# Performance work log

Measured on AMD Instinct MI355X. Metric: run time of the kernel, lower is better.

## Reference

```python
import jax, jax.numpy as jnp
import numpy as np

B, S, D, H = 64, 512, 256, 512

def setup_inputs() -> dict:
    key = jax.random.key(0)
    ks = jax.random.split(key, 16)
    s_in = 1.0 / np.sqrt(D)
    s_h = 1.0 / np.sqrt(H)
    inp = {
        "inputs": jax.random.normal(ks[0], (B, S, D), jnp.float32),
        # input-side gate weights (stored [D,H], equiv to torch Linear weight.T)
        "Wf": jax.random.uniform(ks[1], (D, H), jnp.float32, -s_in, s_in),
        "Wi": jax.random.uniform(ks[2], (D, H), jnp.float32, -s_in, s_in),
        "Wo": jax.random.uniform(ks[3], (D, H), jnp.float32, -s_in, s_in),
        "Wc": jax.random.uniform(ks[4], (D, H), jnp.float32, -s_in, s_in),
        "bf": jax.random.uniform(ks[5], (H,), jnp.float32, -s_in, s_in),
        "bi": jax.random.uniform(ks[6], (H,), jnp.float32, -s_in, s_in),
        "bo": jax.random.uniform(ks[7], (H,), jnp.float32, -s_in, s_in),
        "bc": jax.random.uniform(ks[8], (H,), jnp.float32, -s_in, s_in),
        # recurrent weights (bias=False)
        "Uf": jax.random.uniform(ks[9], (H, H), jnp.float32, -s_h, s_h),
        "Ui": jax.random.uniform(ks[10], (H, H), jnp.float32, -s_h, s_h),
        "Uo": jax.random.uniform(ks[11], (H, H), jnp.float32, -s_h, s_h),
        "Uc": jax.random.uniform(ks[12], (H, H), jnp.float32, -s_h, s_h),
        # output head
        "Wfc": jax.random.uniform(ks[13], (H, 1), jnp.float32, -s_h, s_h),
        "bfc": jax.random.uniform(ks[14], (1,), jnp.float32, -s_h, s_h),
    }
    return inp


def reference(inputs, Wf, Wi, Wo, Wc, bf, bi, bo, bc, Uf, Ui, Uo, Uc, Wfc, bfc):
    # Precompute all input-side gate projections in one big GEMM: [B,S,4H]
    Wx = jnp.concatenate([Wf, Wi, Wo, Wc], axis=1)            # [D,4H]
    bx = jnp.concatenate([bf, bi, bo, bc], axis=0)            # [4H]
    gx = jnp.einsum('bsd,dg->bsg', inputs, Wx) + bx           # [B,S,4H]
    Uh = jnp.concatenate([Uf, Ui, Uo, Uc], axis=1)            # [H,4H]

    h0 = jnp.zeros((inputs.shape[0], Uf.shape[0]), inputs.dtype)
    c0 = jnp.zeros_like(h0)
    Hd = Uf.shape[0]

    def step(carry, gx_t):
        h, c = carry
        g = gx_t + h @ Uh                                     # [B,4H]
        f_t = jax.nn.sigmoid(g[:, 0 * Hd:1 * Hd])
        i_t = jax.nn.sigmoid(g[:, 1 * Hd:2 * Hd])
        o_t = jax.nn.sigmoid(g[:, 2 * Hd:3 * Hd])
        chat = jnp.tanh(g[:, 3 * Hd:4 * Hd])
        c = f_t * c + i_t * chat
        h = o_t * jnp.tanh(c)
        return (h, c), h

    (h_t, c_t), hs = jax.lax.scan(step, (h0, c0), jnp.swapaxes(gx, 0, 1))
    outputs = jnp.swapaxes(hs, 0, 1)                          # [B,S,H]
    predictions = jnp.einsum('bsh,ho->bso', outputs, Wfc) + bfc
    return predictions, h_t, c_t
```

## Files before the change

### kernel.cpp

```cpp
#include <hip/hip_runtime.h>
#include <hip/hip_bf16.h>

#define B_ 64
#define S_ 512
#define D_ 256
#define H_ 512

typedef __attribute__((ext_vector_type(8))) short bf16x8;
typedef __attribute__((ext_vector_type(4))) float f32x4;
typedef __attribute__((ext_vector_type(4))) unsigned int uint4v;
typedef unsigned short ushort_t;
typedef unsigned long long u64_t;

__device__ __forceinline__ ushort_t f2bf(float f) {
    __hip_bfloat16 h = __float2bfloat16(f);
    return *reinterpret_cast<ushort_t*>(&h);
}
__device__ __forceinline__ float sigmoid_f(float x) { return 1.f / (1.f + __expf(-x)); }
__device__ __forceinline__ float tanh_f(float x) { return 1.f - 2.f / (__expf(2.f * x) + 1.f); }

__device__ __forceinline__ void lds_barrier() {
    asm volatile("s_waitcnt lgkmcnt(0)\n\ts_barrier" ::: "memory");
}

__global__ __launch_bounds__(512, 2) void lstm_rec(
    const float* __restrict__ X,
    const float* __restrict__ Wf, const float* __restrict__ Wi,
    const float* __restrict__ Wo, const float* __restrict__ Wc,
    const float* __restrict__ bfp, const float* __restrict__ bip,
    const float* __restrict__ bop, const float* __restrict__ bcp,
    const float* __restrict__ Uf, const float* __restrict__ Ui,
    const float* __restrict__ Uo, const float* __restrict__ Uc,
    const float* __restrict__ Wfc,
    float* __restrict__ pred, u64_t* __restrict__ hbuf,
    unsigned int* __restrict__ xcdtab,
    float* __restrict__ outH, float* __restrict__ outC)
{
    __shared__ ushort_t hS[16 * 520];
    __shared__ ushort_t xS[16 * 264];
    __shared__ float gact[4][16][68];
    __shared__ int meta[2];

    const int tid  = threadIdx.x;
    const int w    = tid >> 6;
    const int lane = tid & 63;
    const int q    = lane >> 4;
    const int m    = lane & 15;
    const int gate = w >> 1;
    const int half = w & 1;

    if (w == 0) {
        unsigned int xcd;
        asm volatile("s_getreg_b32 %0, hwreg(HW_REG_XCC_ID)" : "=s"(xcd));
        xcd &= 15u;
        if (lane == 0)
            __hip_atomic_store(&xcdtab[blockIdx.x], xcd + 1u,
                               __ATOMIC_RELEASE, __HIP_MEMORY_SCOPE_AGENT);
        unsigned int entry;
        for (;;) {
            entry = __hip_atomic_load(&xcdtab[lane], __ATOMIC_ACQUIRE, __HIP_MEMORY_SCOPE_AGENT);
            if (__ballot(entry != 0u) == ~0ull) break;
            __builtin_amdgcn_s_sleep(1);
        }
        const unsigned int xcd_j = entry - 1u;
        const unsigned int key_j = (xcd_j << 8) | (unsigned int)lane;
        const unsigned int mykey = (xcd << 8) | (unsigned int)blockIdx.x;
        const int rank = __popcll(__ballot(key_j < mykey));
        const int c_lt = __popcll(__ballot(xcd_j < xcd));
        const int c_eq = __popcll(__ballot(xcd_j == xcd));
        const int gg   = rank >> 3;
        const bool uni = (c_lt <= gg * 8) && (gg * 8 + 8 <= c_lt + c_eq);
        if (lane == 0) { meta[0] = rank; meta[1] = uni ? 1 : 0; }
    }
    __syncthreads();
    const int  rank    = meta[0];
    const bool uniform = meta[1] != 0;
    if (rank >= 32) return;
    const int g = rank >> 3;
    const int s = rank & 7;

    const int ncol0 = s * 64 + half * 32 + m;
    const int ncol1 = ncol0 + 16;

    const float* Ug = (gate == 0) ? Uf : (gate == 1) ? Ui : (gate == 2) ? Uo : Uc;
    const float* Wg = (gate == 0) ? Wf : (gate == 1) ? Wi : (gate == 2) ? Wo : Wc;
    const float* bg = (gate == 0) ? bfp : (gate == 1) ? bip : (gate == 2) ? bop : bcp;

    const float bias0 = bg[ncol0];
    const float bias1 = bg[ncol1];

    bf16x8 UF[2][16];
    bf16x8 WF[2][8];
    #pragma unroll
    for (int tt = 0; tt < 2; ++tt) {
        const int nc = tt ? ncol1 : ncol0;
        #pragma unroll
        for (int ks = 0; ks < 16; ++ks) {
            bf16x8 v;
            #pragma unroll
            for (int j = 0; j < 8; ++j)
                v[j] = (short)f2bf(Ug[(ks * 32 + q * 8 + j) * H_ + nc]);
            UF[tt][ks] = v;
        }
        #pragma unroll
        for (int ks = 0; ks < 8; ++ks) {
            bf16x8 v;
            #pragma unroll
            for (int j = 0; j < 8; ++j)
                v[j] = (short)f2bf(Wg[(ks * 32 + q * 8 + j) * H_ + nc]);
            WF[tt][ks] = v;
        }
    }

    const int urow  = tid >> 5;
    const int upair = tid & 31;
    const float2 wfc2 = *(const float2*)&Wfc[s * 64 + 2 * upair];

    float cr0 = 0.f, cr1 = 0.f;

    {
        const float* xsrc = &X[((size_t)(g * 16 + urow) * S_ + 0) * D_ + upair * 8];
        float4 a = *(const float4*)xsrc;
        float4 b = *(const float4*)(xsrc + 4);
        bf16x8 v;
        v[0] = (short)f2bf(a.x); v[1] = (short)f2bf(a.y);
        v[2] = (short)f2bf(a.z); v[3] = (short)f2bf(a.w);
        v[4] = (short)f2bf(b.x); v[5] = (short)f2bf(b.y);
        v[6] = (short)f2bf(b.z); v[7] = (short)f2bf(b.w);
        *(bf16x8*)&xS[urow * 264 + upair * 8] = v;
    }

    float4 xr0, xr1;

    for (int t = 0; t < S_; ++t) {
        {
            const int row = tid >> 5;
            const int pr  = (tid & 31) * 8;
            u64_t* pe = hbuf + ((size_t)((t & 1) * B_ + g * 16 + row) * 256 + pr);
            const unsigned int tg = (unsigned int)t;
            uint4v ra, rb;
            bool got = false;
            if (uniform) {
                uint4v r0, r1, r2, r3;
                asm volatile(
                    "global_load_dwordx4 %0, %4, off sc0\n\t"
                    "global_load_dwordx4 %1, %5, off sc0\n\t"
                    "global_load_dwordx4 %2, %6, off sc0\n\t"
                    "global_load_dwordx4 %3, %7, off sc0\n\t"
                    "s_waitcnt vmcnt(0)"
                    : "=v"(r0), "=v"(r1), "=v"(r2), "=v"(r3)
                    : "v"(pe), "v"(pe + 2), "v"(pe + 4), "v"(pe + 6)
                    : "memory");
                bool ok = r0[1] == tg && r0[3] == tg && r1[1] == tg && r1[3] == tg
                       && r2[1] == tg && r2[3] == tg && r3[1] == tg && r3[3] == tg;
                if (__ballot(ok) == ~0ull) {
                    ra[0] = r0[0]; ra[1] = r0[2]; ra[2] = r1[0]; ra[3] = r1[2];
                    rb[0] = r2[0]; rb[1] = r2[2]; rb[2] = r3[0]; rb[3] = r3[2];
                    got = true;
                }
            }
            if (!got) {
                for (;;) {
                    u64_t e0 = __hip_atomic_load(pe + 0, __ATOMIC_RELAXED, __HIP_MEMORY_SCOPE_AGENT);
                    u64_t e1 = __hip_atomic_load(pe + 1, __ATOMIC_RELAXED, __HIP_MEMORY_SCOPE_AGENT);
                    u64_t e2 = __hip_atomic_load(pe + 2, __ATOMIC_RELAXED, __HIP_MEMORY_SCOPE_AGENT);
                    u64_t e3 = __hip_atomic_load(pe + 3, __ATOMIC_RELAXED, __HIP_MEMORY_SCOPE_AGENT);
                    u64_t e4 = __hip_atomic_load(pe + 4, __ATOMIC_RELAXED, __HIP_MEMORY_SCOPE_AGENT);
                    u64_t e5 = __hip_atomic_load(pe + 5, __ATOMIC_RELAXED, __HIP_MEMORY_SCOPE_AGENT);
                    u64_t e6 = __hip_atomic_load(pe + 6, __ATOMIC_RELAXED, __HIP_MEMORY_SCOPE_AGENT);
                    u64_t e7 = __hip_atomic_load(pe + 7, __ATOMIC_RELAXED, __HIP_MEMORY_SCOPE_AGENT);
                    bool ok = (unsigned int)(e0 >> 32) == tg && (unsigned int)(e1 >> 32) == tg
                           && (unsigned int)(e2 >> 32) == tg && (unsigned int)(e3 >> 32) == tg
                           && (unsigned int)(e4 >> 32) == tg && (unsigned int)(e5 >> 32) == tg
                           && (unsigned int)(e6 >> 32) == tg && (unsigned int)(e7 >> 32) == tg;
                    if (__ballot(ok) == ~0ull) {
                        ra[0] = (unsigned int)e0; ra[1] = (unsigned int)e1;
                        ra[2] = (unsigned int)e2; ra[3] = (unsigned int)e3;
                        rb[0] = (unsigned int)e4; rb[1] = (unsigned int)e5;
                        rb[2] = (unsigned int)e6; rb[3] = (unsigned int)e7;
                        break;
                    }
                    __builtin_amdgcn_s_sleep(1);
                }
            }
            if (t + 1 < S_) {
                const float* xsrc = &X[((size_t)(g * 16 + urow) * S_ + (t + 1)) * D_ + upair * 8];
                xr0 = *(const float4*)xsrc;
                xr1 = *(const float4*)(xsrc + 4);
            }
            *(uint4v*)&hS[row * 520 + pr * 2]     = ra;
            *(uint4v*)&hS[row * 520 + pr * 2 + 8] = rb;
        }
        lds_barrier();

        f32x4 accA0 = {bias0, bias0, bias0, bias0};
        f32x4 accA1 = {bias1, bias1, bias1, bias1};
        f32x4 accB0 = {0.f, 0.f, 0.f, 0.f};
        f32x4 accB1 = {0.f, 0.f, 0.f, 0.f};
        #pragma unroll
        for (int ks = 0; ks < 8; ++ks) {
            bf16x8 a = *(const bf16x8*)&xS[m * 264 + ks * 32 + q * 8];
            accA0 = __builtin_amdgcn_mfma_f32_16x16x32_bf16(a, WF[0][ks], accA0, 0, 0, 0);
            accA1 = __builtin_amdgcn_mfma_f32_16x16x32_bf16(a, WF[1][ks], accA1, 0, 0, 0);
        }
        #pragma unroll
        for (int ks = 0; ks < 16; ++ks) {
            bf16x8 a = *(const bf16x8*)&hS[m * 520 + ks * 32 + q * 8];
            accB0 = __builtin_amdgcn_mfma_f32_16x16x32_bf16(a, UF[0][ks], accB0, 0, 0, 0);
            accB1 = __builtin_amdgcn_mfma_f32_16x16x32_bf16(a, UF[1][ks], accB1, 0, 0, 0);
        }
        #pragma unroll
        for (int j = 0; j < 4; ++j) {
            float v0 = accA0[j] + accB0[j];
            float v1 = accA1[j] + accB1[j];
            v0 = (gate < 3) ? sigmoid_f(v0) : tanh_f(v0);
            v1 = (gate < 3) ? sigmoid_f(v1) : tanh_f(v1);
            gact[gate][q * 4 + j][half * 32 + m]      = v0;
            gact[gate][q * 4 + j][half * 32 + 16 + m] = v1;
        }
        lds_barrier();

        float2 f2v = *(const float2*)&gact[0][urow][2 * upair];
        float2 i2v = *(const float2*)&gact[1][urow][2 * upair];
        float2 o2v = *(const float2*)&gact[2][urow][2 * upair];
        float2 ch2 = *(const float2*)&gact[3][urow][2 * upair];
        cr0 = f2v.x * cr0 + i2v.x * ch2.x;
        cr1 = f2v.y * cr1 + i2v.y * ch2.y;
        float hv0 = o2v.x * tanh_f(cr0);
        float hv1 = o2v.y * tanh_f(cr1);

        if (t < S_ - 1) {
            unsigned int packed = (unsigned int)f2bf(hv0) | ((unsigned int)f2bf(hv1) << 16);
            u64_t ent = ((u64_t)(unsigned int)(t + 1) << 32) | (u64_t)packed;
            u64_t* hdst = hbuf + ((size_t)(((t + 1) & 1) * B_ + g * 16 + urow) * 256
                                  + s * 32 + upair);
            asm volatile("global_store_dwordx2 %0, %1, off sc0 sc1"
                         :: "v"(hdst), "v"(ent) : "memory");
            bf16x8 v;
            v[0] = (short)f2bf(xr0.x); v[1] = (short)f2bf(xr0.y);
            v[2] = (short)f2bf(xr0.z); v[3] = (short)f2bf(xr0.w);
            v[4] = (short)f2bf(xr1.x); v[5] = (short)f2bf(xr1.y);
            v[6] = (short)f2bf(xr1.z); v[7] = (short)f2bf(xr1.w);
            *(bf16x8*)&xS[urow * 264 + upair * 8] = v;
        } else {
            *(float2*)&outH[(g * 16 + urow) * H_ + s * 64 + 2 * upair] = make_float2(hv0, hv1);
            *(float2*)&outC[(g * 16 + urow) * H_ + s * 64 + 2 * upair] = make_float2(cr0, cr1);
        }

        float pv = hv0 * wfc2.x + hv1 * wfc2.y;
        pv += __shfl_xor(pv, 16);
        pv += __shfl_xor(pv, 8);
        pv += __shfl_xor(pv, 4);
        pv += __shfl_xor(pv, 2);
        pv += __shfl_xor(pv, 1);
        if (upair == 0) atomicAdd(&pred[(g * 16 + urow) * S_ + t], pv);
    }
}

__global__ void pred_fin(const float* __restrict__ pred,
                         const float* __restrict__ bfc,
                         float* __restrict__ out)
{
    int i = blockIdx.x * blockDim.x + threadIdx.x;
    if (i < B_ * S_) out[i] = pred[i] + bfc[0];
}

extern "C" void kernel_launch(void* const* d_in, const int* in_sizes, int n_in,
                              void* d_out, int out_size, void* d_ws, size_t ws_size,
                              hipStream_t stream) {
    const float* X   = (const float*)d_in[0];
    const float* Wf  = (const float*)d_in[1];
    const float* Wi  = (const float*)d_in[2];
    const float* Wo  = (const float*)d_in[3];
    const float* Wc  = (const float*)d_in[4];
    const float* bfp = (const float*)d_in[5];
    const float* bip = (const float*)d_in[6];
    const float* bop = (const float*)d_in[7];
    const float* bcp = (const float*)d_in[8];
    const float* Uf  = (const float*)d_in[9];
    const float* Ui  = (const float*)d_in[10];
    const float* Uo  = (const float*)d_in[11];
    const float* Uc  = (const float*)d_in[12];
    const float* Wfc = (const float*)d_in[13];
    const float* bfc = (const float*)d_in[14];

    float*        pred   = (float*)d_ws;
    u64_t*        hbuf   = (u64_t*)((char*)d_ws + 131072);
    unsigned int* xcdtab = (unsigned int*)((char*)d_ws + 393216);

    hipMemsetAsync(d_ws, 0, 393216 + 256, stream);

    float* out = (float*)d_out;
    lstm_rec<<<64, 512, 0, stream>>>(X, Wf, Wi, Wo, Wc, bfp, bip, bop, bcp,
                                     Uf, Ui, Uo, Uc, Wfc,
                                     pred, hbuf, xcdtab,
                                     out + 32768, out + 65536);
    pred_fin<<<128, 256, 0, stream>>>(pred, bfc, out);
}
```

Measured before the change: 2.231 ms.

## Process all four batch groups per block on eight co-located blocks

Instead of 32 active blocks (4 batch groups × 8 hidden slices), only 8 blocks stay active and each loops over all four 16-row batch groups per timestep, with separate LDS buffers per group. The intent is to keep all cooperating blocks on one XCD so cross-block h exchange stays in a shared cache and the fast uniform load path is taken more often. In exchange each block does four times the serial work per step with more barriers, and the uniform flag now requires the eight lowest-ranked blocks to share the lowest XCD.

```diff
diff --git a/kernel.cpp b/kernel.cpp
--- a/kernel.cpp
+++ b/kernel.cpp
@@ -23,7 +23,7 @@
     asm volatile("s_waitcnt lgkmcnt(0)\n\ts_barrier" ::: "memory");
 }
 
-__global__ __launch_bounds__(512, 2) void lstm_rec(
+__global__ __launch_bounds__(512) void lstm_rec(
     const float* __restrict__ X,
     const float* __restrict__ Wf, const float* __restrict__ Wi,
     const float* __restrict__ Wo, const float* __restrict__ Wc,
@@ -36,9 +36,8 @@
     unsigned int* __restrict__ xcdtab,
     float* __restrict__ outH, float* __restrict__ outC)
 {
-    __shared__ ushort_t hS[16 * 520];
-    __shared__ ushort_t xS[16 * 264];
-    __shared__ float gact[4][16][68];
+    __shared__ __attribute__((aligned(16))) unsigned char blob[4][17408];
+    __shared__ ushort_t xS[4][16 * 264];
     __shared__ int meta[2];
 
     const int tid  = threadIdx.x;
@@ -68,16 +67,14 @@
         const int rank = __popcll(__ballot(key_j < mykey));
         const int c_lt = __popcll(__ballot(xcd_j < xcd));
         const int c_eq = __popcll(__ballot(xcd_j == xcd));
-        const int gg   = rank >> 3;
-        const bool uni = (c_lt <= gg * 8) && (gg * 8 + 8 <= c_lt + c_eq);
+        const bool uni = (c_lt == 0) && (c_eq >= 8);
         if (lane == 0) { meta[0] = rank; meta[1] = uni ? 1 : 0; }
     }
     __syncthreads();
     const int  rank    = meta[0];
     const bool uniform = meta[1] != 0;
-    if (rank >= 32) return;
-    const int g = rank >> 3;
-    const int s = rank & 7;
+    if (rank >= 8) return;
+    const int s = rank;
 
     const int ncol0 = s * 64 + half * 32 + m;
     const int ncol1 = ncol0 + 16;
@@ -116,10 +113,12 @@
     const int upair = tid & 31;
     const float2 wfc2 = *(const float2*)&Wfc[s * 64 + 2 * upair];
 
-    float cr0 = 0.f, cr1 = 0.f;
-
-    {
-        const float* xsrc = &X[((size_t)(g * 16 + urow) * S_ + 0) * D_ + upair * 8];
+    float cr0[4] = {0.f, 0.f, 0.f, 0.f};
+    float cr1[4] = {0.f, 0.f, 0.f, 0.f};
+
+    #pragma unroll
+    for (int gi = 0; gi < 4; ++gi) {
+        const float* xsrc = &X[((size_t)(gi * 16 + urow) * S_ + 0) * D_ + upair * 8];
         float4 a = *(const float4*)xsrc;
         float4 b = *(const float4*)(xsrc + 4);
         bf16x8 v;
@@ -127,133 +126,140 @@
         v[2] = (short)f2bf(a.z); v[3] = (short)f2bf(a.w);
         v[4] = (short)f2bf(b.x); v[5] = (short)f2bf(b.y);
         v[6] = (short)f2bf(b.z); v[7] = (short)f2bf(b.w);
-        *(bf16x8*)&xS[urow * 264 + upair * 8] = v;
+        *(bf16x8*)&xS[gi][urow * 264 + upair * 8] = v;
     }
 
-    float4 xr0, xr1;
-
     for (int t = 0; t < S_; ++t) {
-        {
-            const int row = tid >> 5;
-            const int pr  = (tid & 31) * 8;
-            u64_t* pe = hbuf + ((size_t)((t & 1) * B_ + g * 16 + row) * 256 + pr);
-            const unsigned int tg = (unsigned int)t;
-            uint4v ra, rb;
-            bool got = false;
-            if (uniform) {
-                uint4v r0, r1, r2, r3;
-                asm volatile(
-                    "global_load_dwordx4 %0, %4, off sc0\n\t"
-                    "global_load_dwordx4 %1, %5, off sc0\n\t"
-                    "global_load_dwordx4 %2, %6, off sc0\n\t"
-                    "global_load_dwordx4 %3, %7, off sc0\n\t"
-                    "s_waitcnt vmcnt(0)"
-                    : "=v"(r0), "=v"(r1), "=v"(r2), "=v"(r3)
-                    : "v"(pe), "v"(pe + 2), "v"(pe + 4), "v"(pe + 6)
-                    : "memory");
-                bool ok = r0[1] == tg && r0[3] == tg && r1[1] == tg && r1[3] == tg
-                       && r2[1] == tg && r2[3] == tg && r3[1] == tg && r3[3] == tg;
-                if (__ballot(ok) == ~0ull) {
-                    ra[0] = r0[0]; ra[1] = r0[2]; ra[2] = r1[0]; ra[3] = r1[2];
-                    rb[0] = r2[0]; rb[1] = r2[2]; rb[2] = r3[0]; rb[3] = r3[2];
-                    got = true;
+        #pragma unroll
+        for (int gi = 0; gi < 4; ++gi) {
+            ushort_t* hS = (ushort_t*)blob[gi];
+            float*    ga = (float*)blob[gi];
+            float4 xr0, xr1;
+
+            {
+                const int row = tid >> 5;
+                const int pr  = (tid & 31) * 8;
+                u64_t* pe = hbuf + ((size_t)((t & 1) * B_ + gi * 16 + row) * 256 + pr);
+                const unsigned int tg = (unsigned int)t;
+                uint4v ra, rb;
+                bool got = false;
+                if (uniform) {
+                    uint4v r0, r1, r2, r3;
+                    asm volatile(
+                        "global_load_dwordx4 %0, %4, off sc0\n\t"
+                        "global_load_dwordx4 %1, %5, off sc0\n\t"
+                        "global_load_dwordx4 %2, %6, off sc0\n\t"
+                        "global_load_dwordx4 %3, %7, off sc0\n\t"
+                        "s_waitcnt vmcnt(0)"
+                        : "=v"(r0), "=v"(r1), "=v"(r2), "=v"(r3)
+                        : "v"(pe), "v"(pe + 2), "v"(pe + 4), "v"(pe + 6)
+                        : "memory");
+                    bool ok = r0[1] == tg && r0[3] == tg && r1[1] == tg && r1[3] == tg
+                           && r2[1] == tg && r2[3] == tg && r3[1] == tg && r3[3] == tg;
+                    if (__ballot(ok) == ~0ull) {
+                        ra[0] = r0[0]; ra[1] = r0[2]; ra[2] = r1[0]; ra[3] = r1[2];
+                        rb[0] = r2[0]; rb[1] = r2[2]; rb[2] = r3[0]; rb[3] = r3[2];
+                        got = true;
+                    }
                 }
-            }
-            if (!got) {
-                for (;;) {
-                    u64_t e0 = __hip_atomic_load(pe + 0, __ATOMIC_RELAXED, __HIP_MEMORY_SCOPE_AGENT);
-                    u64_t e1 = __hip_atomic_load(pe + 1, __ATOMIC_RELAXED, __HIP_MEMORY_SCOPE_AGENT);
-                    u64_t e2 = __hip_atomic_load(pe + 2, __ATOMIC_RELAXED, __HIP_MEMORY_SCOPE_AGENT);
-                    u64_t e3 = __hip_atomic_load(pe + 3, __ATOMIC_RELAXED, __HIP_MEMORY_SCOPE_AGENT);
-                    u64_t e4 = __hip_atomic_load(pe + 4, __ATOMIC_RELAXED, __HIP_MEMORY_SCOPE_AGENT);
-                    u64_t e5 = __hip_atomic_load(pe + 5, __ATOMIC_RELAXED, __HIP_MEMORY_SCOPE_AGENT);
-                    u64_t e6 = __hip_atomic_load(pe + 6, __ATOMIC_RELAXED, __HIP_MEMORY_SCOPE_AGENT);
-                    u64_t e7 = __hip_atomic_load(pe + 7, __ATOMIC_RELAXED, __HIP_MEMORY_SCOPE_AGENT);
-                    bool ok = (unsigned int)(e0 >> 32) == tg && (unsigned int)(e1 >> 32) == tg
-                           && (unsigned int)(e2 >> 32) == tg && (unsigned int)(e3 >> 32) == tg
-                           && (unsigned int)(e4 >> 32) == tg && (unsigned int)(e5 >> 32) == tg
-                           && (unsigned int)(e6 >> 32) == tg && (unsigned int)(e7 >> 32) == tg;
-                    if (__ballot(ok) == ~0ull) {
-                        ra[0] = (unsigned int)e0; ra[1] = (unsigned int)e1;
-                        ra[2] = (unsigned int)e2; ra[3] = (unsigned int)e3;
-                        rb[0] = (unsigned int)e4; rb[1] = (unsigned int)e5;
-                        rb[2] = (unsigned int)e6; rb[3] = (unsigned int)e7;
-                        break;
+                if (!got) {
+                    for (;;) {
+                        u64_t e0 = __hip_atomic_load(pe + 0, __ATOMIC_RELAXED, __HIP_MEMORY_SCOPE_AGENT);
+                        u64_t e1 = __hip_atomic_load(pe + 1, __ATOMIC_RELAXED, __HIP_MEMORY_SCOPE_AGENT);
+                        u64_t e2 = __hip_atomic_load(pe + 2, __ATOMIC_RELAXED, __HIP_MEMORY_SCOPE_AGENT);
+                        u64_t e3 = __hip_atomic_load(pe + 3, __ATOMIC_RELAXED, __HIP_MEMORY_SCOPE_AGENT);
+                        u64_t e4 = __hip_atomic_load(pe + 4, __ATOMIC_RELAXED, __HIP_MEMORY_SCOPE_AGENT);
+                        u64_t e5 = __hip_atomic_load(pe + 5, __ATOMIC_RELAXED, __HIP_MEMORY_SCOPE_AGENT);
+                        u64_t e6 = __hip_atomic_load(pe + 6, __ATOMIC_RELAXED, __HIP_MEMORY_SCOPE_AGENT);
+                        u64_t e7 = __hip_atomic_load(pe + 7, __ATOMIC_RELAXED, __HIP_MEMORY_SCOPE_AGENT);
+                        bool ok = (unsigned int)(e0 >> 32) == tg && (unsigned int)(e1 >> 32) == tg
+                               && (unsigned int)(e2 >> 32) == tg && (unsigned int)(e3 >> 32) == tg
+                               && (unsigned int)(e4 >> 32) == tg && (unsigned int)(e5 >> 32) == tg
+                               && (unsigned int)(e6 >> 32) == tg && (unsigned int)(e7 >> 32) == tg;
+                        if (__ballot(ok) == ~0ull) {
+                            ra[0] = (unsigned int)e0; ra[1] = (unsigned int)e1;
+                            ra[2] = (unsigned int)e2; ra[3] = (unsigned int)e3;
+                            rb[0] = (unsigned int)e4; rb[1] = (unsigned int)e5;
+                            rb[2] = (unsigned int)e6; rb[3] = (unsigned int)e7;
+                            break;
+                        }
+                        __builtin_amdgcn_s_sleep(1);
                     }
-                    __builtin_amdgcn_s_sleep(1);
                 }
-            }
-            if (t + 1 < S_) {
-                const float* xsrc = &X[((size_t)(g * 16 + urow) * S_ + (t + 1)) * D_ + upair * 8];
-                xr0 = *(const float4*)xsrc;
-                xr1 = *(const float4*)(xsrc + 4);
-            }
-            *(uint4v*)&hS[row * 520 + pr * 2]     = ra;
-            *(uint4v*)&hS[row * 520 + pr * 2 + 8] = rb;
+                if (t + 1 < S_) {
+                    const float* xs2 = &X[((size_t)(gi * 16 + urow) * S_ + (t + 1)) * D_ + upair * 8];
+                    xr0 = *(const float4*)xs2;
+                    xr1 = *(const float4*)(xs2 + 4);
+                }
+                *(uint4v*)&hS[row * 520 + pr * 2]     = ra;
+                *(uint4v*)&hS[row * 520 + pr * 2 + 8] = rb;
+            }
+            lds_barrier();
+
+            f32x4 accA0 = {bias0, bias0, bias0, bias0};
+            f32x4 accA1 = {bias1, bias1, bias1, bias1};
+            f32x4 accB0 = {0.f, 0.f, 0.f, 0.f};
+            f32x4 accB1 = {0.f, 0.f, 0.f, 0.f};
+            #pragma unroll
+            for (int ks = 0; ks < 8; ++ks) {
+                bf16x8 a = *(const bf16x8*)&xS[gi][m * 264 + ks * 32 + q * 8];
+                accA0 = __builtin_amdgcn_mfma_f32_16x16x32_bf16(a, WF[0][ks], accA0, 0, 0, 0);
+                accA1 = __builtin_amdgcn_mfma_f32_16x16x32_bf16(a, WF[1][ks], accA1, 0, 0, 0);
+            }
+            #pragma unroll
+            for (int ks = 0; ks < 16; ++ks) {
+                bf16x8 a = *(const bf16x8*)&hS[m * 520 + ks * 32 + q * 8];
+                accB0 = __builtin_amdgcn_mfma_f32_16x16x32_bf16(a, UF[0][ks], accB0, 0, 0, 0);
+                accB1 = __builtin_amdgcn_mfma_f32_16x16x32_bf16(a, UF[1][ks], accB1, 0, 0, 0);
+            }
+            lds_barrier();
+
+            #pragma unroll
+            for (int j = 0; j < 4; ++j) {
+                float v0 = accA0[j] + accB0[j];
+                float v1 = accA1[j] + accB1[j];
+                v0 = (gate < 3) ? sigmoid_f(v0) : tanh_f(v0);
+                v1 = (gate < 3) ? sigmoid_f(v1) : tanh_f(v1);
+                ga[((size_t)gate * 16 + q * 4 + j) * 68 + half * 32 + m]      = v0;
+                ga[((size_t)gate * 16 + q * 4 + j) * 68 + half * 32 + 16 + m] = v1;
+            }
+            lds_barrier();
+
+            float2 f2v = *(const float2*)&ga[((size_t)0 * 16 + urow) * 68 + 2 * upair];
+            float2 i2v = *(const float2*)&ga[((size_t)1 * 16 + urow) * 68 + 2 * upair];
+            float2 o2v = *(const float2*)&ga[((size_t)2 * 16 + urow) * 68 + 2 * upair];
+            float2 ch2 = *(const float2*)&ga[((size_t)3 * 16 + urow) * 68 + 2 * upair];
+            cr0[gi] = f2v.x * cr0[gi] + i2v.x * ch2.x;
+            cr1[gi] = f2v.y * cr1[gi] + i2v.y * ch2.y;
+            float hv0 = o2v.x * tanh_f(cr0[gi]);
+            float hv1 = o2v.y * tanh_f(cr1[gi]);
+
+            if (t < S_ - 1) {
+                unsigned int packed = (unsigned int)f2bf(hv0) | ((unsigned int)f2bf(hv1) << 16);
+                u64_t ent = ((u64_t)(unsigned int)(t + 1) << 32) | (u64_t)packed;
+                u64_t* hdst = hbuf + ((size_t)(((t + 1) & 1) * B_ + gi * 16 + urow) * 256
+                                      + s * 32 + upair);
+                asm volatile("global_store_dwordx2 %0, %1, off sc0 sc1"
+                             :: "v"(hdst), "v"(ent) : "memory");
+                bf16x8 v;
+                v[0] = (short)f2bf(xr0.x); v[1] = (short)f2bf(xr0.y);
+                v[2] = (short)f2bf(xr0.z); v[3] = (short)f2bf(xr0.w);
+                v[4] = (short)f2bf(xr1.x); v[5] = (short)f2bf(xr1.y);
+                v[6] = (short)f2bf(xr1.z); v[7] = (short)f2bf(xr1.w);
+                *(bf16x8*)&xS[gi][urow * 264 + upair * 8] = v;
+            } else {
+                *(float2*)&outH[(gi * 16 + urow) * H_ + s * 64 + 2 * upair] = make_float2(hv0, hv1);
+                *(float2*)&outC[(gi * 16 + urow) * H_ + s * 64 + 2 * upair] = make_float2(cr0[gi], cr1[gi]);
+            }
+
+            float pv = hv0 * wfc2.x + hv1 * wfc2.y;
+            pv += __shfl_xor(pv, 16);
+            pv += __shfl_xor(pv, 8);
+            pv += __shfl_xor(pv, 4);
+            pv += __shfl_xor(pv, 2);
+            pv += __shfl_xor(pv, 1);
+            if (upair == 0) atomicAdd(&pred[(gi * 16 + urow) * S_ + t], pv);
         }
-        lds_barrier();
-
-        f32x4 accA0 = {bias0, bias0, bias0, bias0};
-        f32x4 accA1 = {bias1, bias1, bias1, bias1};
-        f32x4 accB0 = {0.f, 0.f, 0.f, 0.f};
-        f32x4 accB1 = {0.f, 0.f, 0.f, 0.f};
-        #pragma unroll
-        for (int ks = 0; ks < 8; ++ks) {
-            bf16x8 a = *(const bf16x8*)&xS[m * 264 + ks * 32 + q * 8];
-            accA0 = __builtin_amdgcn_mfma_f32_16x16x32_bf16(a, WF[0][ks], accA0, 0, 0, 0);
-            accA1 = __builtin_amdgcn_mfma_f32_16x16x32_bf16(a, WF[1][ks], accA1, 0, 0, 0);
-        }
-        #pragma unroll
-        for (int ks = 0; ks < 16; ++ks) {
-            bf16x8 a = *(const bf16x8*)&hS[m * 520 + ks * 32 + q * 8];
-            accB0 = __builtin_amdgcn_mfma_f32_16x16x32_bf16(a, UF[0][ks], accB0, 0, 0, 0);
-            accB1 = __builtin_amdgcn_mfma_f32_16x16x32_bf16(a, UF[1][ks], accB1, 0, 0, 0);
-        }
-        #pragma unroll
-        for (int j = 0; j < 4; ++j) {
-            float v0 = accA0[j] + accB0[j];
-            float v1 = accA1[j] + accB1[j];
-            v0 = (gate < 3) ? sigmoid_f(v0) : tanh_f(v0);
-            v1 = (gate < 3) ? sigmoid_f(v1) : tanh_f(v1);
-            gact[gate][q * 4 + j][half * 32 + m]      = v0;
-            gact[gate][q * 4 + j][half * 32 + 16 + m] = v1;
-        }
-        lds_barrier();
-
-        float2 f2v = *(const float2*)&gact[0][urow][2 * upair];
-        float2 i2v = *(const float2*)&gact[1][urow][2 * upair];
-        float2 o2v = *(const float2*)&gact[2][urow][2 * upair];
-        float2 ch2 = *(const float2*)&gact[3][urow][2 * upair];
-        cr0 = f2v.x * cr0 + i2v.x * ch2.x;
-        cr1 = f2v.y * cr1 + i2v.y * ch2.y;
-        float hv0 = o2v.x * tanh_f(cr0);
-        float hv1 = o2v.y * tanh_f(cr1);
-
-        if (t < S_ - 1) {
-            unsigned int packed = (unsigned int)f2bf(hv0) | ((unsigned int)f2bf(hv1) << 16);
-            u64_t ent = ((u64_t)(unsigned int)(t + 1) << 32) | (u64_t)packed;
-            u64_t* hdst = hbuf + ((size_t)(((t + 1) & 1) * B_ + g * 16 + urow) * 256
-                                  + s * 32 + upair);
-            asm volatile("global_store_dwordx2 %0, %1, off sc0 sc1"
-                         :: "v"(hdst), "v"(ent) : "memory");
-            bf16x8 v;
-            v[0] = (short)f2bf(xr0.x); v[1] = (short)f2bf(xr0.y);
-            v[2] = (short)f2bf(xr0.z); v[3] = (short)f2bf(xr0.w);
-            v[4] = (short)f2bf(xr1.x); v[5] = (short)f2bf(xr1.y);
-            v[6] = (short)f2bf(xr1.z); v[7] = (short)f2bf(xr1.w);
-            *(bf16x8*)&xS[urow * 264 + upair * 8] = v;
-        } else {
-            *(float2*)&outH[(g * 16 + urow) * H_ + s * 64 + 2 * upair] = make_float2(hv0, hv1);
-            *(float2*)&outC[(g * 16 + urow) * H_ + s * 64 + 2 * upair] = make_float2(cr0, cr1);
-        }
-
-        float pv = hv0 * wfc2.x + hv1 * wfc2.y;
-        pv += __shfl_xor(pv, 16);
-        pv += __shfl_xor(pv, 8);
-        pv += __shfl_xor(pv, 4);
-        pv += __shfl_xor(pv, 2);
-        pv += __shfl_xor(pv, 1);
-        if (upair == 0) atomicAdd(&pred[(g * 16 + urow) * S_ + t], pv);
     }
 }
 
@@ -288,7 +294,7 @@
     u64_t*        hbuf   = (u64_t*)((char*)d_ws + 131072);
     unsigned int* xcdtab = (unsigned int*)((char*)d_ws + 393216);
 
-    hipMemsetAsync(d_ws, 0, 393216 + 256, stream);
+    hipMemsetAsync(d_ws, 0, 393472, stream);
 
     float* out = (float*)d_out;
     lstm_rec<<<64, 512, 0, stream>>>(X, Wf, Wi, Wo, Wc, bfp, bip, bop, bcp,
```

Measured after the change: 8.847 ms. 3.97x slower.
